# Kernel tuning notes

Measured on AMD Instinct MI355X. Metric: run time of the kernel, lower is better.

## Reference

```python
import jax, jax.numpy as jnp
import numpy as np

N_NODES = 100000
N_EDGES = 800000
F_IN = 128
C_HID = 32
N_CLS = 16
K_HOPS = 3
CST = 1e-05


def setup_inputs() -> dict:
    key = jax.random.key(0)
    ks = jax.random.split(key, 12)
    node_feat = jax.random.normal(ks[0], (N_NODES, F_IN), dtype=jnp.float32)
    edge_index = jax.random.randint(ks[1], (2, N_EDGES), 0, N_NODES, dtype=jnp.int64)
    def lin(k, fan_in, fan_out):
        bound = 1.0 / np.sqrt(fan_in)
        kw, kb = jax.random.split(k)
        W = jax.random.uniform(kw, (fan_in, fan_out), minval=-bound, maxval=bound, dtype=jnp.float32)
        b = jax.random.uniform(kb, (fan_out,), minval=-bound, maxval=bound, dtype=jnp.float32)
        return W, b
    W_in, b_in = lin(ks[2], F_IN, C_HID)
    Wq, bq = lin(ks[3], C_HID, C_HID)
    Wk, bk = lin(ks[4], C_HID, C_HID)
    Wv, bv = lin(ks[5], C_HID, N_CLS)
    hopwise = jnp.ones((K_HOPS + 1,), dtype=jnp.float32)
    return {"node_feat": node_feat, "edge_index": edge_index,
            "W_in": W_in, "b_in": b_in, "Wq": Wq, "bq": bq,
            "Wk": Wk, "bk": bk, "Wv": Wv, "bv": bv, "hopwise": hopwise}


def reference(node_feat, edge_index, W_in, b_in, Wq, bq, Wk, bk, Wv, bv, hopwise):
    n = node_feat.shape[0]
    row, col = edge_index[0], edge_index[1]  # messages flow row -> col (PyG source_to_target)
    x = jax.nn.relu(node_feat @ W_in + b_in)            # [n, c]
    Q = 1.0 + jax.nn.elu(x @ Wq + bq)                    # [n, c]
    K = 1.0 + jax.nn.elu(x @ Wk + bk)                    # [n, c]
    V = x @ Wv + bv                                      # [n, d]
    M = jnp.einsum('ni,nj->nij', K, V)                   # [n, c, d]
    hidden = V * hopwise[0]
    for hop in range(K_HOPS):
        # scatter-sum aggregation over edges (aggr='add')
        M = jax.ops.segment_sum(M[row], col, num_segments=n)  # [n, c, d]
        K = jax.ops.segment_sum(K[row], col, num_segments=n)  # [n, c]
        H = jnp.einsum('ni,nij->nj', Q, M)               # [n, d]
        C = jnp.einsum('ni,ni->n', Q, K)[:, None] + CST  # [n, 1]
        hidden = hidden + hopwise[hop + 1] * (H / C)
    return hidden
```

## Files before the change

kernel.cpp:

```cpp
#include <hip/hip_runtime.h>
#include <math.h>

#define NN 100000
#define NE 800000
#define F_IN 128
#define CH 32
#define NC 16
#define CSTF 1e-5f
#define CAP 48
#define PBLK 2048
#define PSTRIDE (PBLK * 4)

typedef float v2f __attribute__((ext_vector_type(2)));
typedef float v4f __attribute__((ext_vector_type(4)));
typedef short v8s __attribute__((ext_vector_type(8)));

__device__ __forceinline__ float bf_lo(unsigned int u) {
    unsigned int t = u << 16;
    return __builtin_bit_cast(float, t);
}
__device__ __forceinline__ float bf_hi(unsigned int u) {
    unsigned int t = u & 0xffff0000u;
    return __builtin_bit_cast(float, t);
}
__device__ __forceinline__ float bf_val(unsigned short v) {
    unsigned int t = ((unsigned int)v) << 16;
    return __builtin_bit_cast(float, t);
}
__device__ __forceinline__ v2f bf_pair(unsigned int u) {
    v2f r; r.x = bf_lo(u); r.y = bf_hi(u); return r;
}
__device__ __forceinline__ unsigned int bf_round(float a) {
    unsigned int ua = __builtin_bit_cast(unsigned int, a);
    return (ua + 0x7fffu + ((ua >> 16) & 1u)) >> 16;
}
__device__ __forceinline__ short bfq(float a) {
    unsigned int ua = __builtin_bit_cast(unsigned int, a);
    return (short)((ua + 0x8000u) >> 16);
}
__device__ __forceinline__ unsigned int bf_pack2(float a, float b) {
    return bf_round(a) | (bf_round(b) << 16);
}

__device__ __forceinline__ float cl448(float a) {
    return fminf(fmaxf(a, -448.f), 448.f);
}

__device__ __forceinline__ float elu1(float x) {
    return 1.f + ((x > 0.f) ? x : (expf(x) - 1.f));
}

__device__ __forceinline__ int get_row(const int* ei, int e, int m) {
    return m ? ei[2 * e] : ei[e];
}
__device__ __forceinline__ int get_col(const int* ei, int e, int m) {
    return m ? ei[2 * NE + 2 * e] : ei[NE + e];
}

__global__ void fillb_kernel(const int* __restrict__ ei, int* __restrict__ deg,
                             int* __restrict__ srcs) {
    __shared__ int smode;
    int nz = 0;
    if (threadIdx.x < 64) nz = (ei[2 * threadIdx.x + 1] != 0) ? 1 : 0;
    unsigned long long b = __ballot(nz);
    if (threadIdx.x == 0) smode = (b == 0ULL) ? 1 : 0;
    __syncthreads();
    int m = smode;
    int e = blockIdx.x * 256 + threadIdx.x;
    if (e < NE) {
        int c = get_col(ei, e, m);
        int p = atomicAdd(&deg[c], 1);
        if (p < CAP) srcs[(size_t)c * CAP + p] = get_row(ei, e, m);
    }
}

__global__ __launch_bounds__(256) void phase1_kernel(
    const float* __restrict__ feat, const float* __restrict__ Win,
    const float* __restrict__ bin, const float* __restrict__ Wq,
    const float* __restrict__ bq, const float* __restrict__ Wk,
    const float* __restrict__ bk, const float* __restrict__ Wv,
    const float* __restrict__ bv, const float* __restrict__ hopwise,
    float* __restrict__ Qg, unsigned short* __restrict__ Kb,
    unsigned short* __restrict__ Vb, float* __restrict__ out)
{
    __shared__ float xs_all[4][16 * 36];

    int tid  = threadIdx.x;
    int wid  = tid >> 6;
    int lane = tid & 63;
    int q    = lane >> 4;
    int col  = lane & 15;
    int node0 = (blockIdx.x * 4 + wid) * 16;

    v8s wb[4][2];
#pragma unroll
    for (int kk = 0; kk < 4; ++kk)
#pragma unroll
        for (int t = 0; t < 2; ++t)
#pragma unroll
            for (int j = 0; j < 8; ++j)
                wb[kk][t][j] = (short)bf_round(Win[(kk * 32 + q * 8 + j) * CH + t * 16 + col]);

    v8s wq[2], wk[2], wv;
#pragma unroll
    for (int t = 0; t < 2; ++t)
#pragma unroll
        for (int j = 0; j < 8; ++j) {
            wq[t][j] = (short)bf_round(Wq[(q * 8 + j) * CH + t * 16 + col]);
            wk[t][j] = (short)bf_round(Wk[(q * 8 + j) * CH + t * 16 + col]);
        }
#pragma unroll
    for (int j = 0; j < 8; ++j)
        wv[j] = (short)bf_round(Wv[(q * 8 + j) * NC + col]);

    float bin0 = bin[col], bin1 = bin[col + 16];
    float bq0 = bq[col], bq1 = bq[col + 16];
    float bk0 = bk[col], bk1 = bk[col + 16];
    float bv0 = bv[col];
    float hw0 = hopwise[0];

    int nodeA = node0 + col;
    int nclamp = nodeA < NN ? nodeA : NN - 1;
    const float* fr = feat + (size_t)nclamp * F_IN + q * 8;

    v4f acc0 = {0.f, 0.f, 0.f, 0.f}, acc1 = {0.f, 0.f, 0.f, 0.f};
#pragma unroll
    for (int kk = 0; kk < 4; ++kk) {
        float4 a = *(const float4*)(fr + kk * 32);
        float4 b = *(const float4*)(fr + kk * 32 + 4);
        v8s af;
        af[0] = bfq(a.x); af[1] = bfq(a.y); af[2] = bfq(a.z); af[3] = bfq(a.w);
        af[4] = bfq(b.x); af[5] = bfq(b.y); af[6] = bfq(b.z); af[7] = bfq(b.w);
        acc0 = __builtin_amdgcn_mfma_f32_16x16x32_bf16(af, wb[kk][0], acc0, 0, 0, 0);
        acc1 = __builtin_amdgcn_mfma_f32_16x16x32_bf16(af, wb[kk][1], acc1, 0, 0, 0);
    }

    float* xs = xs_all[wid];
#pragma unroll
    for (int r = 0; r < 4; ++r) {
        xs[(q * 4 + r) * 36 + col]      = fmaxf(acc0[r] + bin0, 0.f);
        xs[(q * 4 + r) * 36 + col + 16] = fmaxf(acc1[r] + bin1, 0.f);
    }

    float4 xa = *(const float4*)&xs[col * 36 + q * 8];
    float4 xb = *(const float4*)&xs[col * 36 + q * 8 + 4];
    v8s xf;
    xf[0] = bfq(xa.x); xf[1] = bfq(xa.y); xf[2] = bfq(xa.z); xf[3] = bfq(xa.w);
    xf[4] = bfq(xb.x); xf[5] = bfq(xb.y); xf[6] = bfq(xb.z); xf[7] = bfq(xb.w);

    v4f aq0 = {0.f,0.f,0.f,0.f}, aq1 = {0.f,0.f,0.f,0.f};
    v4f ak0 = {0.f,0.f,0.f,0.f}, ak1 = {0.f,0.f,0.f,0.f};
    v4f av  = {0.f,0.f,0.f,0.f};
    aq0 = __builtin_amdgcn_mfma_f32_16x16x32_bf16(xf, wq[0], aq0, 0, 0, 0);
    aq1 = __builtin_amdgcn_mfma_f32_16x16x32_bf16(xf, wq[1], aq1, 0, 0, 0);
    ak0 = __builtin_amdgcn_mfma_f32_16x16x32_bf16(xf, wk[0], ak0, 0, 0, 0);
    ak1 = __builtin_amdgcn_mfma_f32_16x16x32_bf16(xf, wk[1], ak1, 0, 0, 0);
    av  = __builtin_amdgcn_mfma_f32_16x16x32_bf16(xf, wv,    av,  0, 0, 0);

#pragma unroll
    for (int r = 0; r < 4; ++r) {
        int nd = node0 + 4 * q + r;
        if (nd < NN) {
            float q0 = elu1(aq0[r] + bq0);
            float q1 = elu1(aq1[r] + bq1);
            float k0 = elu1(ak0[r] + bk0);
            float k1 = elu1(ak1[r] + bk1);
            float vv = av[r] + bv0;
            Qg[(size_t)nd * CH + col]      = q0;
            Qg[(size_t)nd * CH + col + 16] = q1;
            Kb[(size_t)nd * CH + col]      = (unsigned short)bf_round(k0);
            Kb[(size_t)nd * CH + col + 16] = (unsigned short)bf_round(k1);
            Vb[(size_t)nd * NC + col]      = (unsigned short)bf_round(vv);
            out[(size_t)nd * NC + col]     = hw0 * vv;
        }
    }
}

__global__ __launch_bounds__(256) void hopA_kernel(
    const float* __restrict__ Qg, const unsigned short* __restrict__ Kb,
    const unsigned short* __restrict__ Vb,
    unsigned char* __restrict__ Mout, unsigned short* __restrict__ Kout,
    const int* __restrict__ deg, const int* __restrict__ srcs,
    const float* __restrict__ hopw, float* __restrict__ out)
{
    int tid  = threadIdx.x;
    int wid  = tid >> 6;
    int lane = tid & 63;
    int jB   = lane >> 2;
    int s4   = lane & 3;
    int cseg = s4 * 8;
    float hw = hopw[1];

    int node = __builtin_amdgcn_readfirstlane(blockIdx.x * 4 + wid);
    int d = deg[node];

    while (true) {
        int node_nx = node + PSTRIDE;
        int d_nx = 0;
        if (node_nx < NN) d_nx = deg[node_nx];

        if (d > CAP) d = CAP;
        const int* sl = srcs + (size_t)node * CAP;

        const float4* qp = (const float4*)(Qg + (size_t)node * CH + cseg);
        float4 qa = qp[0], qb = qp[1];

        v2f acc2[4];
#pragma unroll
        for (int t = 0; t < 4; ++t) { acc2[t].x = 0.f; acc2[t].y = 0.f; }
        v2f kagg2[4];
#pragma unroll
        for (int t = 0; t < 4; ++t) { kagg2[t].x = 0.f; kagg2[t].y = 0.f; }

        int i = 0;
        for (; i + 3 < d; i += 4) {
            int s0 = sl[i], s1 = sl[i+1], s2 = sl[i+2], s3 = sl[i+3];
            uint4 kr0 = *(const uint4*)(Kb + (size_t)s0 * CH + cseg);
            uint4 kr1 = *(const uint4*)(Kb + (size_t)s1 * CH + cseg);
            uint4 kr2 = *(const uint4*)(Kb + (size_t)s2 * CH + cseg);
            uint4 kr3 = *(const uint4*)(Kb + (size_t)s3 * CH + cseg);
            float vj0 = bf_val(Vb[(size_t)s0 * NC + jB]);
            float vj1 = bf_val(Vb[(size_t)s1 * NC + jB]);
            float vj2 = bf_val(Vb[(size_t)s2 * NC + jB]);
            float vj3 = bf_val(Vb[(size_t)s3 * NC + jB]);
            v2f k;
            k = bf_pair(kr0.x); kagg2[0] += k; acc2[0] += k * vj0;
            k = bf_pair(kr0.y); kagg2[1] += k; acc2[1] += k * vj0;
            k = bf_pair(kr0.z); kagg2[2] += k; acc2[2] += k * vj0;
            k = bf_pair(kr0.w); kagg2[3] += k; acc2[3] += k * vj0;
            k = bf_pair(kr1.x); kagg2[0] += k; acc2[0] += k * vj1;
            k = bf_pair(kr1.y); kagg2[1] += k; acc2[1] += k * vj1;
            k = bf_pair(kr1.z); kagg2[2] += k; acc2[2] += k * vj1;
            k = bf_pair(kr1.w); kagg2[3] += k; acc2[3] += k * vj1;
            k = bf_pair(kr2.x); kagg2[0] += k; acc2[0] += k * vj2;
            k = bf_pair(kr2.y); kagg2[1] += k; acc2[1] += k * vj2;
            k = bf_pair(kr2.z); kagg2[2] += k; acc2[2] += k * vj2;
            k = bf_pair(kr2.w); kagg2[3] += k; acc2[3] += k * vj2;
            k = bf_pair(kr3.x); kagg2[0] += k; acc2[0] += k * vj3;
            k = bf_pair(kr3.y); kagg2[1] += k; acc2[1] += k * vj3;
            k = bf_pair(kr3.z); kagg2[2] += k; acc2[2] += k * vj3;
            k = bf_pair(kr3.w); kagg2[3] += k; acc2[3] += k * vj3;
        }
        for (; i < d; ++i) {
            int s0 = sl[i];
            uint4 kr0 = *(const uint4*)(Kb + (size_t)s0 * CH + cseg);
            float vj0 = bf_val(Vb[(size_t)s0 * NC + jB]);
            v2f k;
            k = bf_pair(kr0.x); kagg2[0] += k; acc2[0] += k * vj0;
            k = bf_pair(kr0.y); kagg2[1] += k; acc2[1] += k * vj0;
            k = bf_pair(kr0.z); kagg2[2] += k; acc2[2] += k * vj0;
            k = bf_pair(kr0.w); kagg2[3] += k; acc2[3] += k * vj0;
        }

        v2f q2[4];
        q2[0].x = qa.x; q2[0].y = qa.y; q2[1].x = qa.z; q2[1].y = qa.w;
        q2[2].x = qb.x; q2[2].y = qb.y; q2[3].x = qb.z; q2[3].y = qb.w;

        v2f t = q2[0] * kagg2[0] + q2[1] * kagg2[1]
              + q2[2] * kagg2[2] + q2[3] * kagg2[3];
        float cpv = t.x + t.y;
        cpv += __shfl_xor(cpv, 1);
        cpv += __shfl_xor(cpv, 2);
        float sc = hw / (cpv + CSTF);

        if (lane < 4) {
            uint4 kw;
            kw.x = bf_pack2(kagg2[0].x, kagg2[0].y);
            kw.y = bf_pack2(kagg2[1].x, kagg2[1].y);
            kw.z = bf_pack2(kagg2[2].x, kagg2[2].y);
            kw.w = bf_pack2(kagg2[3].x, kagg2[3].y);
            *(uint4*)(Kout + (size_t)node * CH + cseg) = kw;
        }
        int p0 = 0, p1 = 0;
        p0 = __builtin_amdgcn_cvt_pk_fp8_f32(cl448(acc2[0].x), cl448(acc2[0].y), p0, false);
        p0 = __builtin_amdgcn_cvt_pk_fp8_f32(cl448(acc2[1].x), cl448(acc2[1].y), p0, true);
        p1 = __builtin_amdgcn_cvt_pk_fp8_f32(cl448(acc2[2].x), cl448(acc2[2].y), p1, false);
        p1 = __builtin_amdgcn_cvt_pk_fp8_f32(cl448(acc2[3].x), cl448(acc2[3].y), p1, true);
        uint2 u; u.x = (unsigned int)p0; u.y = (unsigned int)p1;
        *(uint2*)(Mout + (size_t)node * 512 + lane * 8) = u;

        v2f h2 = q2[0] * acc2[0] + q2[1] * acc2[1]
               + q2[2] * acc2[2] + q2[3] * acc2[3];
        float hp = h2.x + h2.y;
        hp += __shfl_xor(hp, 1);
        hp += __shfl_xor(hp, 2);

        if (s4 == 0)
            out[(size_t)node * NC + jB] += sc * hp;

        if (node_nx >= NN) break;
        node = node_nx;
        d = d_nx;
    }
}

template<bool WRITE>
__global__ __launch_bounds__(256) void hopM_kernel(
    const float* __restrict__ Qg, const unsigned short* __restrict__ Kb,
    const unsigned char* __restrict__ Min,
    unsigned char* __restrict__ Mout, unsigned short* __restrict__ Kout,
    const int* __restrict__ deg, const int* __restrict__ srcs,
    const float* __restrict__ hopw, int hop, float* __restrict__ out)
{
    int tid  = threadIdx.x;
    int wid  = tid >> 6;
    int lane = tid & 63;
    int jB   = lane >> 2;
    int s4   = lane & 3;
    int cseg = s4 * 8;
    int c32  = lane & 31;
    float hw = hopw[hop];

    int node = __builtin_amdgcn_readfirstlane(blockIdx.x * 4 + wid);
    int d = deg[node];

    while (true) {
        int node_nx = node + PSTRIDE;
        int d_nx = 0;
        if (node_nx < NN) d_nx = deg[node_nx];

        if (d > CAP) d = CAP;
        const int* sl = srcs + (size_t)node * CAP;

        float qcl = Qg[(size_t)node * CH + c32];
        const float4* qp = (const float4*)(Qg + (size_t)node * CH + cseg);
        float4 qa = qp[0], qb = qp[1];

        v2f acc2[4];
#pragma unroll
        for (int t = 0; t < 4; ++t) { acc2[t].x = 0.f; acc2[t].y = 0.f; }
        float kagg = 0.f;

        int i = 0;
        for (; i + 3 < d; i += 4) {
            int s0 = sl[i], s1 = sl[i+1], s2 = sl[i+2], s3 = sl[i+3];
            uint2 u0 = *(const uint2*)(Min + (size_t)s0 * 512 + lane * 8);
            uint2 u1 = *(const uint2*)(Min + (size_t)s1 * 512 + lane * 8);
            uint2 u2 = *(const uint2*)(Min + (size_t)s2 * 512 + lane * 8);
            uint2 u3 = *(const uint2*)(Min + (size_t)s3 * 512 + lane * 8);
            float k0 = bf_val(Kb[(size_t)s0 * CH + c32]);
            float k1 = bf_val(Kb[(size_t)s1 * CH + c32]);
            float k2 = bf_val(Kb[(size_t)s2 * CH + c32]);
            float k3 = bf_val(Kb[(size_t)s3 * CH + c32]);
            kagg += (k0 + k1) + (k2 + k3);
            acc2[0] += (v2f)__builtin_amdgcn_cvt_pk_f32_fp8(u0.x, false);
            acc2[1] += (v2f)__builtin_amdgcn_cvt_pk_f32_fp8(u0.x, true);
            acc2[2] += (v2f)__builtin_amdgcn_cvt_pk_f32_fp8(u0.y, false);
            acc2[3] += (v2f)__builtin_amdgcn_cvt_pk_f32_fp8(u0.y, true);
            acc2[0] += (v2f)__builtin_amdgcn_cvt_pk_f32_fp8(u1.x, false);
            acc2[1] += (v2f)__builtin_amdgcn_cvt_pk_f32_fp8(u1.x, true);
            acc2[2] += (v2f)__builtin_amdgcn_cvt_pk_f32_fp8(u1.y, false);
            acc2[3] += (v2f)__builtin_amdgcn_cvt_pk_f32_fp8(u1.y, true);
            acc2[0] += (v2f)__builtin_amdgcn_cvt_pk_f32_fp8(u2.x, false);
            acc2[1] += (v2f)__builtin_amdgcn_cvt_pk_f32_fp8(u2.x, true);
            acc2[2] += (v2f)__builtin_amdgcn_cvt_pk_f32_fp8(u2.y, false);
            acc2[3] += (v2f)__builtin_amdgcn_cvt_pk_f32_fp8(u2.y, true);
            acc2[0] += (v2f)__builtin_amdgcn_cvt_pk_f32_fp8(u3.x, false);
            acc2[1] += (v2f)__builtin_amdgcn_cvt_pk_f32_fp8(u3.x, true);
            acc2[2] += (v2f)__builtin_amdgcn_cvt_pk_f32_fp8(u3.y, false);
            acc2[3] += (v2f)__builtin_amdgcn_cvt_pk_f32_fp8(u3.y, true);
        }
        for (; i < d; ++i) {
            int s0 = sl[i];
            uint2 u0 = *(const uint2*)(Min + (size_t)s0 * 512 + lane * 8);
            kagg += bf_val(Kb[(size_t)s0 * CH + c32]);
            acc2[0] += (v2f)__builtin_amdgcn_cvt_pk_f32_fp8(u0.x, false);
            acc2[1] += (v2f)__builtin_amdgcn_cvt_pk_f32_fp8(u0.x, true);
            acc2[2] += (v2f)__builtin_amdgcn_cvt_pk_f32_fp8(u0.y, false);
            acc2[3] += (v2f)__builtin_amdgcn_cvt_pk_f32_fp8(u0.y, true);
        }

        float cpv = qcl * kagg;
#pragma unroll
        for (int st = 1; st <= 16; st <<= 1) cpv += __shfl_xor(cpv, st);
        float sc = hw / (cpv + CSTF);

        if (WRITE) {
            if (lane < 32)
                Kout[(size_t)node * CH + c32] = (unsigned short)bf_round(kagg);
            int p0 = 0, p1 = 0;
            p0 = __builtin_amdgcn_cvt_pk_fp8_f32(cl448(acc2[0].x), cl448(acc2[0].y), p0, false);
            p0 = __builtin_amdgcn_cvt_pk_fp8_f32(cl448(acc2[1].x), cl448(acc2[1].y), p0, true);
            p1 = __builtin_amdgcn_cvt_pk_fp8_f32(cl448(acc2[2].x), cl448(acc2[2].y), p1, false);
            p1 = __builtin_amdgcn_cvt_pk_fp8_f32(cl448(acc2[3].x), cl448(acc2[3].y), p1, true);
            uint2 u; u.x = (unsigned int)p0; u.y = (unsigned int)p1;
            *(uint2*)(Mout + (size_t)node * 512 + lane * 8) = u;
        }

        v2f q2[4];
        q2[0].x = qa.x; q2[0].y = qa.y; q2[1].x = qa.z; q2[1].y = qa.w;
        q2[2].x = qb.x; q2[2].y = qb.y; q2[3].x = qb.z; q2[3].y = qb.w;
        v2f h2 = q2[0] * acc2[0] + q2[1] * acc2[1]
               + q2[2] * acc2[2] + q2[3] * acc2[3];
        float hp = h2.x + h2.y;
        hp += __shfl_xor(hp, 1);
        hp += __shfl_xor(hp, 2);

        if (s4 == 0)
            out[(size_t)node * NC + jB] += sc * hp;

        if (node_nx >= NN) break;
        node = node_nx;
        d = d_nx;
    }
}

extern "C" void kernel_launch(void* const* d_in, const int* in_sizes, int n_in,
                              void* d_out, int out_size, void* d_ws, size_t ws_size,
                              hipStream_t stream) {
    const float* feat = (const float*)d_in[0];
    const int*   ei   = (const int*)d_in[1];
    const float* Win  = (const float*)d_in[2];
    const float* bin  = (const float*)d_in[3];
    const float* Wq   = (const float*)d_in[4];
    const float* bq   = (const float*)d_in[5];
    const float* Wk   = (const float*)d_in[6];
    const float* bk   = (const float*)d_in[7];
    const float* Wv   = (const float*)d_in[8];
    const float* bv   = (const float*)d_in[9];
    const float* hopw = (const float*)d_in[10];
    float* out = (float*)d_out;

    char* ws = (char*)d_ws;
    size_t off = 0;
    auto alloc = [&](size_t bytes) -> void* {
        void* p = ws + off;
        off += (bytes + 255) & ~(size_t)255;
        return p;
    };
    float*          Qg  = (float*)alloc((size_t)NN * CH * 4);
    unsigned short* K0b = (unsigned short*)alloc((size_t)NN * CH * 2);
    unsigned short* K1b = (unsigned short*)alloc((size_t)NN * CH * 2);
    unsigned short* K2b = (unsigned short*)alloc((size_t)NN * CH * 2);
    unsigned short* Vb  = (unsigned short*)alloc((size_t)NN * NC * 2);
    int*   deg  = (int*)alloc((size_t)NN * 4);
    int*   srcs = (int*)alloc((size_t)NN * CAP * 4);
    unsigned char* MA = (unsigned char*)alloc((size_t)NN * 512);
    unsigned char* MB = (unsigned char*)alloc((size_t)NN * 512);

    hipMemsetAsync(deg, 0, (size_t)NN * 4, stream);
    fillb_kernel<<<(NE + 255) / 256, 256, 0, stream>>>(ei, deg, srcs);

    phase1_kernel<<<1563, 256, 0, stream>>>(feat, Win, bin, Wq, bq, Wk, bk, Wv, bv,
                                            hopw, Qg, K0b, Vb, out);

    hopA_kernel<<<PBLK, 256, 0, stream>>>(Qg, K0b, Vb, MA, K1b, deg, srcs, hopw, out);
    hopM_kernel<true ><<<PBLK, 256, 0, stream>>>(Qg, K1b, MA, MB, K2b, deg, srcs, hopw, 2, out);
    hopM_kernel<false><<<PBLK, 256, 0, stream>>>(Qg, K2b, MB, nullptr, nullptr, deg, srcs, hopw, 3, out);
}
```

Before: 426.1 us.

## Fuse edge fill with phase1 and launch one wave per node in hop kernels

Merges the edge-bucketing kernel and the dense projection kernel into a single launch, with block ranges selecting the role, so both run concurrently. The hop kernels drop their persistent grid-stride loop with next-degree prefetch and launch one wavefront per node (25000 blocks). Output accumulation switches to atomicAdd. This trades per-launch overhead and tail effects against losing the prefetch pipelining, adds atomic traffic, and adds a __syncthreads in the phase1 path, which now sits inside a divergent block-role branch.

Result: faster. 383.9 us (-9.9%).

```diff
diff --git a/kernel.cpp b/kernel.cpp
--- a/kernel.cpp
+++ b/kernel.cpp
@@ -8,8 +8,9 @@
 #define NC 16
 #define CSTF 1e-5f
 #define CAP 48
-#define PBLK 2048
-#define PSTRIDE (PBLK * 4)
+
+#define FILL_BLKS ((NE + 255) / 256)
+#define P1_BLKS   1563
 
 typedef float v2f __attribute__((ext_vector_type(2)));
 typedef float v4f __attribute__((ext_vector_type(4)));
@@ -57,24 +58,8 @@
     return m ? ei[2 * NE + 2 * e] : ei[NE + e];
 }
 
-__global__ void fillb_kernel(const int* __restrict__ ei, int* __restrict__ deg,
-                             int* __restrict__ srcs) {
-    __shared__ int smode;
-    int nz = 0;
-    if (threadIdx.x < 64) nz = (ei[2 * threadIdx.x + 1] != 0) ? 1 : 0;
-    unsigned long long b = __ballot(nz);
-    if (threadIdx.x == 0) smode = (b == 0ULL) ? 1 : 0;
-    __syncthreads();
-    int m = smode;
-    int e = blockIdx.x * 256 + threadIdx.x;
-    if (e < NE) {
-        int c = get_col(ei, e, m);
-        int p = atomicAdd(&deg[c], 1);
-        if (p < CAP) srcs[(size_t)c * CAP + p] = get_row(ei, e, m);
-    }
-}
-
-__global__ __launch_bounds__(256) void phase1_kernel(
+__global__ __launch_bounds__(256) void fill_p1_kernel(
+    const int* __restrict__ ei, int* __restrict__ deg, int* __restrict__ srcs,
     const float* __restrict__ feat, const float* __restrict__ Win,
     const float* __restrict__ bin, const float* __restrict__ Wq,
     const float* __restrict__ bq, const float* __restrict__ Wk,
@@ -83,14 +68,32 @@
     float* __restrict__ Qg, unsigned short* __restrict__ Kb,
     unsigned short* __restrict__ Vb, float* __restrict__ out)
 {
+    if (blockIdx.x < FILL_BLKS) {
+        __shared__ int smode;
+        int nz = 0;
+        if (threadIdx.x < 64) nz = (ei[2 * threadIdx.x + 1] != 0) ? 1 : 0;
+        unsigned long long b = __ballot(nz);
+        if (threadIdx.x == 0) smode = (b == 0ULL) ? 1 : 0;
+        __syncthreads();
+        int m = smode;
+        int e = blockIdx.x * 256 + threadIdx.x;
+        if (e < NE) {
+            int c = get_col(ei, e, m);
+            int p = atomicAdd(&deg[c], 1);
+            if (p < CAP) srcs[(size_t)c * CAP + p] = get_row(ei, e, m);
+        }
+        return;
+    }
+
     __shared__ float xs_all[4][16 * 36];
 
+    int bid  = blockIdx.x - FILL_BLKS;
     int tid  = threadIdx.x;
     int wid  = tid >> 6;
     int lane = tid & 63;
     int q    = lane >> 4;
     int col  = lane & 15;
-    int node0 = (blockIdx.x * 4 + wid) * 16;
+    int node0 = (bid * 4 + wid) * 16;
 
     v8s wb[4][2];
 #pragma unroll
@@ -141,6 +144,7 @@
         xs[(q * 4 + r) * 36 + col]      = fmaxf(acc0[r] + bin0, 0.f);
         xs[(q * 4 + r) * 36 + col + 16] = fmaxf(acc1[r] + bin1, 0.f);
     }
+    __syncthreads();
 
     float4 xa = *(const float4*)&xs[col * 36 + q * 8];
     float4 xb = *(const float4*)&xs[col * 36 + q * 8 + 4];
@@ -186,112 +190,99 @@
     int tid  = threadIdx.x;
     int wid  = tid >> 6;
     int lane = tid & 63;
+    int node = __builtin_amdgcn_readfirstlane(blockIdx.x * 4 + wid);
     int jB   = lane >> 2;
     int s4   = lane & 3;
     int cseg = s4 * 8;
-    float hw = hopw[1];
-
-    int node = __builtin_amdgcn_readfirstlane(blockIdx.x * 4 + wid);
+
+    v2f acc2[4];
+#pragma unroll
+    for (int t = 0; t < 4; ++t) { acc2[t].x = 0.f; acc2[t].y = 0.f; }
+    v2f kagg2[4];
+#pragma unroll
+    for (int t = 0; t < 4; ++t) { kagg2[t].x = 0.f; kagg2[t].y = 0.f; }
+
     int d = deg[node];
-
-    while (true) {
-        int node_nx = node + PSTRIDE;
-        int d_nx = 0;
-        if (node_nx < NN) d_nx = deg[node_nx];
-
-        if (d > CAP) d = CAP;
-        const int* sl = srcs + (size_t)node * CAP;
-
-        const float4* qp = (const float4*)(Qg + (size_t)node * CH + cseg);
-        float4 qa = qp[0], qb = qp[1];
-
-        v2f acc2[4];
-#pragma unroll
-        for (int t = 0; t < 4; ++t) { acc2[t].x = 0.f; acc2[t].y = 0.f; }
-        v2f kagg2[4];
-#pragma unroll
-        for (int t = 0; t < 4; ++t) { kagg2[t].x = 0.f; kagg2[t].y = 0.f; }
-
-        int i = 0;
-        for (; i + 3 < d; i += 4) {
-            int s0 = sl[i], s1 = sl[i+1], s2 = sl[i+2], s3 = sl[i+3];
-            uint4 kr0 = *(const uint4*)(Kb + (size_t)s0 * CH + cseg);
-            uint4 kr1 = *(const uint4*)(Kb + (size_t)s1 * CH + cseg);
-            uint4 kr2 = *(const uint4*)(Kb + (size_t)s2 * CH + cseg);
-            uint4 kr3 = *(const uint4*)(Kb + (size_t)s3 * CH + cseg);
-            float vj0 = bf_val(Vb[(size_t)s0 * NC + jB]);
-            float vj1 = bf_val(Vb[(size_t)s1 * NC + jB]);
-            float vj2 = bf_val(Vb[(size_t)s2 * NC + jB]);
-            float vj3 = bf_val(Vb[(size_t)s3 * NC + jB]);
-            v2f k;
-            k = bf_pair(kr0.x); kagg2[0] += k; acc2[0] += k * vj0;
-            k = bf_pair(kr0.y); kagg2[1] += k; acc2[1] += k * vj0;
-            k = bf_pair(kr0.z); kagg2[2] += k; acc2[2] += k * vj0;
-            k = bf_pair(kr0.w); kagg2[3] += k; acc2[3] += k * vj0;
-            k = bf_pair(kr1.x); kagg2[0] += k; acc2[0] += k * vj1;
-            k = bf_pair(kr1.y); kagg2[1] += k; acc2[1] += k * vj1;
-            k = bf_pair(kr1.z); kagg2[2] += k; acc2[2] += k * vj1;
-            k = bf_pair(kr1.w); kagg2[3] += k; acc2[3] += k * vj1;
-            k = bf_pair(kr2.x); kagg2[0] += k; acc2[0] += k * vj2;
-            k = bf_pair(kr2.y); kagg2[1] += k; acc2[1] += k * vj2;
-            k = bf_pair(kr2.z); kagg2[2] += k; acc2[2] += k * vj2;
-            k = bf_pair(kr2.w); kagg2[3] += k; acc2[3] += k * vj2;
-            k = bf_pair(kr3.x); kagg2[0] += k; acc2[0] += k * vj3;
-            k = bf_pair(kr3.y); kagg2[1] += k; acc2[1] += k * vj3;
-            k = bf_pair(kr3.z); kagg2[2] += k; acc2[2] += k * vj3;
-            k = bf_pair(kr3.w); kagg2[3] += k; acc2[3] += k * vj3;
-        }
-        for (; i < d; ++i) {
-            int s0 = sl[i];
-            uint4 kr0 = *(const uint4*)(Kb + (size_t)s0 * CH + cseg);
-            float vj0 = bf_val(Vb[(size_t)s0 * NC + jB]);
-            v2f k;
-            k = bf_pair(kr0.x); kagg2[0] += k; acc2[0] += k * vj0;
-            k = bf_pair(kr0.y); kagg2[1] += k; acc2[1] += k * vj0;
-            k = bf_pair(kr0.z); kagg2[2] += k; acc2[2] += k * vj0;
-            k = bf_pair(kr0.w); kagg2[3] += k; acc2[3] += k * vj0;
-        }
-
-        v2f q2[4];
-        q2[0].x = qa.x; q2[0].y = qa.y; q2[1].x = qa.z; q2[1].y = qa.w;
-        q2[2].x = qb.x; q2[2].y = qb.y; q2[3].x = qb.z; q2[3].y = qb.w;
-
-        v2f t = q2[0] * kagg2[0] + q2[1] * kagg2[1]
-              + q2[2] * kagg2[2] + q2[3] * kagg2[3];
-        float cpv = t.x + t.y;
-        cpv += __shfl_xor(cpv, 1);
-        cpv += __shfl_xor(cpv, 2);
-        float sc = hw / (cpv + CSTF);
-
-        if (lane < 4) {
-            uint4 kw;
-            kw.x = bf_pack2(kagg2[0].x, kagg2[0].y);
-            kw.y = bf_pack2(kagg2[1].x, kagg2[1].y);
-            kw.z = bf_pack2(kagg2[2].x, kagg2[2].y);
-            kw.w = bf_pack2(kagg2[3].x, kagg2[3].y);
-            *(uint4*)(Kout + (size_t)node * CH + cseg) = kw;
-        }
-        int p0 = 0, p1 = 0;
-        p0 = __builtin_amdgcn_cvt_pk_fp8_f32(cl448(acc2[0].x), cl448(acc2[0].y), p0, false);
-        p0 = __builtin_amdgcn_cvt_pk_fp8_f32(cl448(acc2[1].x), cl448(acc2[1].y), p0, true);
-        p1 = __builtin_amdgcn_cvt_pk_fp8_f32(cl448(acc2[2].x), cl448(acc2[2].y), p1, false);
-        p1 = __builtin_amdgcn_cvt_pk_fp8_f32(cl448(acc2[3].x), cl448(acc2[3].y), p1, true);
-        uint2 u; u.x = (unsigned int)p0; u.y = (unsigned int)p1;
-        *(uint2*)(Mout + (size_t)node * 512 + lane * 8) = u;
-
-        v2f h2 = q2[0] * acc2[0] + q2[1] * acc2[1]
-               + q2[2] * acc2[2] + q2[3] * acc2[3];
-        float hp = h2.x + h2.y;
-        hp += __shfl_xor(hp, 1);
-        hp += __shfl_xor(hp, 2);
-
-        if (s4 == 0)
-            out[(size_t)node * NC + jB] += sc * hp;
-
-        if (node_nx >= NN) break;
-        node = node_nx;
-        d = d_nx;
-    }
+    if (d > CAP) d = CAP;
+    const int* sl = srcs + (size_t)node * CAP;
+    int i = 0;
+
+    for (; i + 3 < d; i += 4) {
+        int s0 = sl[i], s1 = sl[i+1], s2 = sl[i+2], s3 = sl[i+3];
+        uint4 kr0 = *(const uint4*)(Kb + (size_t)s0 * CH + cseg);
+        uint4 kr1 = *(const uint4*)(Kb + (size_t)s1 * CH + cseg);
+        uint4 kr2 = *(const uint4*)(Kb + (size_t)s2 * CH + cseg);
+        uint4 kr3 = *(const uint4*)(Kb + (size_t)s3 * CH + cseg);
+        float vj0 = bf_val(Vb[(size_t)s0 * NC + jB]);
+        float vj1 = bf_val(Vb[(size_t)s1 * NC + jB]);
+        float vj2 = bf_val(Vb[(size_t)s2 * NC + jB]);
+        float vj3 = bf_val(Vb[(size_t)s3 * NC + jB]);
+        v2f k;
+        k = bf_pair(kr0.x); kagg2[0] += k; acc2[0] += k * vj0;
+        k = bf_pair(kr0.y); kagg2[1] += k; acc2[1] += k * vj0;
+        k = bf_pair(kr0.z); kagg2[2] += k; acc2[2] += k * vj0;
+        k = bf_pair(kr0.w); kagg2[3] += k; acc2[3] += k * vj0;
+        k = bf_pair(kr1.x); kagg2[0] += k; acc2[0] += k * vj1;
+        k = bf_pair(kr1.y); kagg2[1] += k; acc2[1] += k * vj1;
+        k = bf_pair(kr1.z); kagg2[2] += k; acc2[2] += k * vj1;
+        k = bf_pair(kr1.w); kagg2[3] += k; acc2[3] += k * vj1;
+        k = bf_pair(kr2.x); kagg2[0] += k; acc2[0] += k * vj2;
+        k = bf_pair(kr2.y); kagg2[1] += k; acc2[1] += k * vj2;
+        k = bf_pair(kr2.z); kagg2[2] += k; acc2[2] += k * vj2;
+        k = bf_pair(kr2.w); kagg2[3] += k; acc2[3] += k * vj2;
+        k = bf_pair(kr3.x); kagg2[0] += k; acc2[0] += k * vj3;
+        k = bf_pair(kr3.y); kagg2[1] += k; acc2[1] += k * vj3;
+        k = bf_pair(kr3.z); kagg2[2] += k; acc2[2] += k * vj3;
+        k = bf_pair(kr3.w); kagg2[3] += k; acc2[3] += k * vj3;
+    }
+    for (; i < d; ++i) {
+        int s0 = sl[i];
+        uint4 kr0 = *(const uint4*)(Kb + (size_t)s0 * CH + cseg);
+        float vj0 = bf_val(Vb[(size_t)s0 * NC + jB]);
+        v2f k;
+        k = bf_pair(kr0.x); kagg2[0] += k; acc2[0] += k * vj0;
+        k = bf_pair(kr0.y); kagg2[1] += k; acc2[1] += k * vj0;
+        k = bf_pair(kr0.z); kagg2[2] += k; acc2[2] += k * vj0;
+        k = bf_pair(kr0.w); kagg2[3] += k; acc2[3] += k * vj0;
+    }
+
+    const float4* qp = (const float4*)(Qg + (size_t)node * CH + cseg);
+    float4 qa = qp[0], qb = qp[1];
+    v2f q2[4];
+    q2[0].x = qa.x; q2[0].y = qa.y; q2[1].x = qa.z; q2[1].y = qa.w;
+    q2[2].x = qb.x; q2[2].y = qb.y; q2[3].x = qb.z; q2[3].y = qb.w;
+
+    v2f t = q2[0] * kagg2[0] + q2[1] * kagg2[1]
+          + q2[2] * kagg2[2] + q2[3] * kagg2[3];
+    float cpv = t.x + t.y;
+    cpv += __shfl_xor(cpv, 1);
+    cpv += __shfl_xor(cpv, 2);
+    float sc = hopw[1] / (cpv + CSTF);
+
+    if (lane < 4) {
+        uint4 kw;
+        kw.x = bf_pack2(kagg2[0].x, kagg2[0].y);
+        kw.y = bf_pack2(kagg2[1].x, kagg2[1].y);
+        kw.z = bf_pack2(kagg2[2].x, kagg2[2].y);
+        kw.w = bf_pack2(kagg2[3].x, kagg2[3].y);
+        *(uint4*)(Kout + (size_t)node * CH + cseg) = kw;
+    }
+    int p0 = 0, p1 = 0;
+    p0 = __builtin_amdgcn_cvt_pk_fp8_f32(cl448(acc2[0].x), cl448(acc2[0].y), p0, false);
+    p0 = __builtin_amdgcn_cvt_pk_fp8_f32(cl448(acc2[1].x), cl448(acc2[1].y), p0, true);
+    p1 = __builtin_amdgcn_cvt_pk_fp8_f32(cl448(acc2[2].x), cl448(acc2[2].y), p1, false);
+    p1 = __builtin_amdgcn_cvt_pk_fp8_f32(cl448(acc2[3].x), cl448(acc2[3].y), p1, true);
+    uint2 u; u.x = (unsigned int)p0; u.y = (unsigned int)p1;
+    *(uint2*)(Mout + (size_t)node * 512 + lane * 8) = u;
+
+    v2f h2 = q2[0] * acc2[0] + q2[1] * acc2[1]
+           + q2[2] * acc2[2] + q2[3] * acc2[3];
+    float hp = h2.x + h2.y;
+    hp += __shfl_xor(hp, 1);
+    hp += __shfl_xor(hp, 2);
+
+    if (s4 == 0)
+        atomicAdd(&out[(size_t)node * NC + jB], sc * hp);
 }
 
 template<bool WRITE>
@@ -305,104 +296,91 @@
     int tid  = threadIdx.x;
     int wid  = tid >> 6;
     int lane = tid & 63;
+    int node = __builtin_amdgcn_readfirstlane(blockIdx.x * 4 + wid);
     int jB   = lane >> 2;
     int s4   = lane & 3;
     int cseg = s4 * 8;
     int c32  = lane & 31;
-    float hw = hopw[hop];
-
-    int node = __builtin_amdgcn_readfirstlane(blockIdx.x * 4 + wid);
+
+    v2f acc2[4];
+#pragma unroll
+    for (int t = 0; t < 4; ++t) { acc2[t].x = 0.f; acc2[t].y = 0.f; }
+    float kagg = 0.f;
+
     int d = deg[node];
-
-    while (true) {
-        int node_nx = node + PSTRIDE;
-        int d_nx = 0;
-        if (node_nx < NN) d_nx = deg[node_nx];
-
-        if (d > CAP) d = CAP;
-        const int* sl = srcs + (size_t)node * CAP;
-
-        float qcl = Qg[(size_t)node * CH + c32];
-        const float4* qp = (const float4*)(Qg + (size_t)node * CH + cseg);
-        float4 qa = qp[0], qb = qp[1];
-
-        v2f acc2[4];
-#pragma unroll
-        for (int t = 0; t < 4; ++t) { acc2[t].x = 0.f; acc2[t].y = 0.f; }
-        float kagg = 0.f;
-
-        int i = 0;
-        for (; i + 3 < d; i += 4) {
-            int s0 = sl[i], s1 = sl[i+1], s2 = sl[i+2], s3 = sl[i+3];
-            uint2 u0 = *(const uint2*)(Min + (size_t)s0 * 512 + lane * 8);
-            uint2 u1 = *(const uint2*)(Min + (size_t)s1 * 512 + lane * 8);
-            uint2 u2 = *(const uint2*)(Min + (size_t)s2 * 512 + lane * 8);
-            uint2 u3 = *(const uint2*)(Min + (size_t)s3 * 512 + lane * 8);
-            float k0 = bf_val(Kb[(size_t)s0 * CH + c32]);
-            float k1 = bf_val(Kb[(size_t)s1 * CH + c32]);
-            float k2 = bf_val(Kb[(size_t)s2 * CH + c32]);
-            float k3 = bf_val(Kb[(size_t)s3 * CH + c32]);
-            kagg += (k0 + k1) + (k2 + k3);
-            acc2[0] += (v2f)__builtin_amdgcn_cvt_pk_f32_fp8(u0.x, false);
-            acc2[1] += (v2f)__builtin_amdgcn_cvt_pk_f32_fp8(u0.x, true);
-            acc2[2] += (v2f)__builtin_amdgcn_cvt_pk_f32_fp8(u0.y, false);
-            acc2[3] += (v2f)__builtin_amdgcn_cvt_pk_f32_fp8(u0.y, true);
-            acc2[0] += (v2f)__builtin_amdgcn_cvt_pk_f32_fp8(u1.x, false);
-            acc2[1] += (v2f)__builtin_amdgcn_cvt_pk_f32_fp8(u1.x, true);
-            acc2[2] += (v2f)__builtin_amdgcn_cvt_pk_f32_fp8(u1.y, false);
-            acc2[3] += (v2f)__builtin_amdgcn_cvt_pk_f32_fp8(u1.y, true);
-            acc2[0] += (v2f)__builtin_amdgcn_cvt_pk_f32_fp8(u2.x, false);
-            acc2[1] += (v2f)__builtin_amdgcn_cvt_pk_f32_fp8(u2.x, true);
-            acc2[2] += (v2f)__builtin_amdgcn_cvt_pk_f32_fp8(u2.y, false);
-            acc2[3] += (v2f)__builtin_amdgcn_cvt_pk_f32_fp8(u2.y, true);
-            acc2[0] += (v2f)__builtin_amdgcn_cvt_pk_f32_fp8(u3.x, false);
-            acc2[1] += (v2f)__builtin_amdgcn_cvt_pk_f32_fp8(u3.x, true);
-            acc2[2] += (v2f)__builtin_amdgcn_cvt_pk_f32_fp8(u3.y, false);
-            acc2[3] += (v2f)__builtin_amdgcn_cvt_pk_f32_fp8(u3.y, true);
-        }
-        for (; i < d; ++i) {
-            int s0 = sl[i];
-            uint2 u0 = *(const uint2*)(Min + (size_t)s0 * 512 + lane * 8);
-            kagg += bf_val(Kb[(size_t)s0 * CH + c32]);
-            acc2[0] += (v2f)__builtin_amdgcn_cvt_pk_f32_fp8(u0.x, false);
-            acc2[1] += (v2f)__builtin_amdgcn_cvt_pk_f32_fp8(u0.x, true);
-            acc2[2] += (v2f)__builtin_amdgcn_cvt_pk_f32_fp8(u0.y, false);
-            acc2[3] += (v2f)__builtin_amdgcn_cvt_pk_f32_fp8(u0.y, true);
-        }
-
-        float cpv = qcl * kagg;
-#pragma unroll
-        for (int st = 1; st <= 16; st <<= 1) cpv += __shfl_xor(cpv, st);
-        float sc = hw / (cpv + CSTF);
-
-        if (WRITE) {
-            if (lane < 32)
-                Kout[(size_t)node * CH + c32] = (unsigned short)bf_round(kagg);
-            int p0 = 0, p1 = 0;
-            p0 = __builtin_amdgcn_cvt_pk_fp8_f32(cl448(acc2[0].x), cl448(acc2[0].y), p0, false);
-            p0 = __builtin_amdgcn_cvt_pk_fp8_f32(cl448(acc2[1].x), cl448(acc2[1].y), p0, true);
-            p1 = __builtin_amdgcn_cvt_pk_fp8_f32(cl448(acc2[2].x), cl448(acc2[2].y), p1, false);
-            p1 = __builtin_amdgcn_cvt_pk_fp8_f32(cl448(acc2[3].x), cl448(acc2[3].y), p1, true);
-            uint2 u; u.x = (unsigned int)p0; u.y = (unsigned int)p1;
-            *(uint2*)(Mout + (size_t)node * 512 + lane * 8) = u;
-        }
-
-        v2f q2[4];
-        q2[0].x = qa.x; q2[0].y = qa.y; q2[1].x = qa.z; q2[1].y = qa.w;
-        q2[2].x = qb.x; q2[2].y = qb.y; q2[3].x = qb.z; q2[3].y = qb.w;
-        v2f h2 = q2[0] * acc2[0] + q2[1] * acc2[1]
-               + q2[2] * acc2[2] + q2[3] * acc2[3];
-        float hp = h2.x + h2.y;
-        hp += __shfl_xor(hp, 1);
-        hp += __shfl_xor(hp, 2);
-
-        if (s4 == 0)
-            out[(size_t)node * NC + jB] += sc * hp;
-
-        if (node_nx >= NN) break;
-        node = node_nx;
-        d = d_nx;
-    }
+    if (d > CAP) d = CAP;
+    const int* sl = srcs + (size_t)node * CAP;
+    int i = 0;
+
+    for (; i + 3 < d; i += 4) {
+        int s0 = sl[i], s1 = sl[i+1], s2 = sl[i+2], s3 = sl[i+3];
+        uint2 u0 = *(const uint2*)(Min + (size_t)s0 * 512 + lane * 8);
+        uint2 u1 = *(const uint2*)(Min + (size_t)s1 * 512 + lane * 8);
+        uint2 u2 = *(const uint2*)(Min + (size_t)s2 * 512 + lane * 8);
+        uint2 u3 = *(const uint2*)(Min + (size_t)s3 * 512 + lane * 8);
+        float k0 = bf_val(Kb[(size_t)s0 * CH + c32]);
+        float k1 = bf_val(Kb[(size_t)s1 * CH + c32]);
+        float k2 = bf_val(Kb[(size_t)s2 * CH + c32]);
+        float k3 = bf_val(Kb[(size_t)s3 * CH + c32]);
+        kagg += (k0 + k1) + (k2 + k3);
+        acc2[0] += (v2f)__builtin_amdgcn_cvt_pk_f32_fp8(u0.x, false);
+        acc2[1] += (v2f)__builtin_amdgcn_cvt_pk_f32_fp8(u0.x, true);
+        acc2[2] += (v2f)__builtin_amdgcn_cvt_pk_f32_fp8(u0.y, false);
+        acc2[3] += (v2f)__builtin_amdgcn_cvt_pk_f32_fp8(u0.y, true);
+        acc2[0] += (v2f)__builtin_amdgcn_cvt_pk_f32_fp8(u1.x, false);
+        acc2[1] += (v2f)__builtin_amdgcn_cvt_pk_f32_fp8(u1.x, true);
+        acc2[2] += (v2f)__builtin_amdgcn_cvt_pk_f32_fp8(u1.y, false);
+        acc2[3] += (v2f)__builtin_amdgcn_cvt_pk_f32_fp8(u1.y, true);
+        acc2[0] += (v2f)__builtin_amdgcn_cvt_pk_f32_fp8(u2.x, false);
+        acc2[1] += (v2f)__builtin_amdgcn_cvt_pk_f32_fp8(u2.x, true);
+        acc2[2] += (v2f)__builtin_amdgcn_cvt_pk_f32_fp8(u2.y, false);
+        acc2[3] += (v2f)__builtin_amdgcn_cvt_pk_f32_fp8(u2.y, true);
+        acc2[0] += (v2f)__builtin_amdgcn_cvt_pk_f32_fp8(u3.x, false);
+        acc2[1] += (v2f)__builtin_amdgcn_cvt_pk_f32_fp8(u3.x, true);
+        acc2[2] += (v2f)__builtin_amdgcn_cvt_pk_f32_fp8(u3.y, false);
+        acc2[3] += (v2f)__builtin_amdgcn_cvt_pk_f32_fp8(u3.y, true);
+    }
+    for (; i < d; ++i) {
+        int s0 = sl[i];
+        uint2 u0 = *(const uint2*)(Min + (size_t)s0 * 512 + lane * 8);
+        kagg += bf_val(Kb[(size_t)s0 * CH + c32]);
+        acc2[0] += (v2f)__builtin_amdgcn_cvt_pk_f32_fp8(u0.x, false);
+        acc2[1] += (v2f)__builtin_amdgcn_cvt_pk_f32_fp8(u0.x, true);
+        acc2[2] += (v2f)__builtin_amdgcn_cvt_pk_f32_fp8(u0.y, false);
+        acc2[3] += (v2f)__builtin_amdgcn_cvt_pk_f32_fp8(u0.y, true);
+    }
+
+    float qcl = Qg[(size_t)node * CH + c32];
+    float cpv = qcl * kagg;
+#pragma unroll
+    for (int st = 1; st <= 16; st <<= 1) cpv += __shfl_xor(cpv, st);
+    float sc = hopw[hop] / (cpv + CSTF);
+
+    if (WRITE) {
+        if (lane < 32)
+            Kout[(size_t)node * CH + c32] = (unsigned short)bf_round(kagg);
+        int p0 = 0, p1 = 0;
+        p0 = __builtin_amdgcn_cvt_pk_fp8_f32(cl448(acc2[0].x), cl448(acc2[0].y), p0, false);
+        p0 = __builtin_amdgcn_cvt_pk_fp8_f32(cl448(acc2[1].x), cl448(acc2[1].y), p0, true);
+        p1 = __builtin_amdgcn_cvt_pk_fp8_f32(cl448(acc2[2].x), cl448(acc2[2].y), p1, false);
+        p1 = __builtin_amdgcn_cvt_pk_fp8_f32(cl448(acc2[3].x), cl448(acc2[3].y), p1, true);
+        uint2 u; u.x = (unsigned int)p0; u.y = (unsigned int)p1;
+        *(uint2*)(Mout + (size_t)node * 512 + lane * 8) = u;
+    }
+
+    const float4* qp = (const float4*)(Qg + (size_t)node * CH + cseg);
+    float4 qa = qp[0], qb = qp[1];
+    v2f q2[4];
+    q2[0].x = qa.x; q2[0].y = qa.y; q2[1].x = qa.z; q2[1].y = qa.w;
+    q2[2].x = qb.x; q2[2].y = qb.y; q2[3].x = qb.z; q2[3].y = qb.w;
+    v2f h2 = q2[0] * acc2[0] + q2[1] * acc2[1]
+           + q2[2] * acc2[2] + q2[3] * acc2[3];
+    float hp = h2.x + h2.y;
+    hp += __shfl_xor(hp, 1);
+    hp += __shfl_xor(hp, 2);
+
+    if (s4 == 0)
+        atomicAdd(&out[(size_t)node * NC + jB], sc * hp);
 }
 
 extern "C" void kernel_launch(void* const* d_in, const int* in_sizes, int n_in,
@@ -439,12 +417,11 @@
     unsigned char* MB = (unsigned char*)alloc((size_t)NN * 512);
 
     hipMemsetAsync(deg, 0, (size_t)NN * 4, stream);
-    fillb_kernel<<<(NE + 255) / 256, 256, 0, stream>>>(ei, deg, srcs);
-
-    phase1_kernel<<<1563, 256, 0, stream>>>(feat, Win, bin, Wq, bq, Wk, bk, Wv, bv,
-                                            hopw, Qg, K0b, Vb, out);
-
-    hopA_kernel<<<PBLK, 256, 0, stream>>>(Qg, K0b, Vb, MA, K1b, deg, srcs, hopw, out);
-    hopM_kernel<true ><<<PBLK, 256, 0, stream>>>(Qg, K1b, MA, MB, K2b, deg, srcs, hopw, 2, out);
-    hopM_kernel<false><<<PBLK, 256, 0, stream>>>(Qg, K2b, MB, nullptr, nullptr, deg, srcs, hopw, 3, out);
-}
+    fill_p1_kernel<<<FILL_BLKS + P1_BLKS, 256, 0, stream>>>(
+        ei, deg, srcs, feat, Win, bin, Wq, bq, Wk, bk, Wv, bv,
+        hopw, Qg, K0b, Vb, out);
+
+    hopA_kernel<<<25000, 256, 0, stream>>>(Qg, K0b, Vb, MA, K1b, deg, srcs, hopw, out);
+    hopM_kernel<true ><<<25000, 256, 0, stream>>>(Qg, K1b, MA, MB, K2b, deg, srcs, hopw, 2, out);
+    hopM_kernel<false><<<25000, 256, 0, stream>>>(Qg, K2b, MB, nullptr, nullptr, deg, srcs, hopw, 3, out);
+}
```
